# Performance work log

Measured on AMD Instinct MI355X. Metric: run time of the kernel, lower is better.

The kernel has to match this reference:

```python
import jax, jax.numpy as jnp
import numpy as np

B, T, D = 4, 1024, 1024
N_HEAD, HEAD, LATENT = 16, 64, 32
N_EXP, TOP_K, N_FF = 8, 2, 4096
HID = int(2 * N_FF / 3)  # 2730, Expert hidden when ffn_multiplier is None
CAP_FACTOR = 1.0


def setup_inputs() -> dict:
    key = jax.random.key(0)
    ks = jax.random.split(key, 14)
    s = 0.02
    f = lambda k, shp: jax.random.normal(k, shp, jnp.float32) * s
    return dict(
        x=jax.random.normal(ks[0], (B, T, D), jnp.float32),
        noise_eps=jax.random.normal(ks[1], (B, T, N_EXP), jnp.float32),
        ln1_w=jnp.ones((D,), jnp.float32),
        ln2_w=jnp.ones((D,), jnp.float32),
        q_w=f(ks[2], (N_HEAD, D, HEAD)), q_b=jnp.zeros((N_HEAD, HEAD), jnp.float32),
        ka_w=f(ks[3], (N_HEAD, D, LATENT)), kb_w=f(ks[4], (N_HEAD, LATENT, HEAD)),
        va_w=f(ks[5], (N_HEAD, D, LATENT)), vb_w=f(ks[6], (N_HEAD, LATENT, HEAD)),
        proj_w=f(ks[7], (D, D)), proj_b=jnp.zeros((D,), jnp.float32),
        route_w=f(ks[8], (D, N_EXP)), route_b=jnp.zeros((N_EXP,), jnp.float32),
        noise_w=f(ks[9], (D, N_EXP)), noise_b=jnp.zeros((N_EXP,), jnp.float32),
        swiglu_w=f(ks[10], (N_EXP, D, 2 * HID)),
        down_w=f(ks[11], (N_EXP, HID, D)),
    )


def _rms(x, w, eps=1e-5):
    x32 = x.astype(jnp.float32)
    n = x32 * jax.lax.rsqrt(jnp.mean(x32 * x32, -1, keepdims=True) + eps)
    return n.astype(x.dtype) * w


def _rope(q, k):
    # q,k: [B,H,T,hd]; even/odd split then concatenated halves (matches torch code)
    hd, Tq = q.shape[-1], q.shape[-2]
    inv = 1.0 / (10000.0 ** (jnp.arange(0, hd, 2, dtype=jnp.float32) / hd))
    ang = jnp.arange(Tq, dtype=jnp.float32)[:, None] * inv[None, :]  # [T, hd/2]
    cos, sin = jnp.cos(ang), jnp.sin(ang)
    def rot(t):
        t1, t2 = t[..., ::2], t[..., 1::2]
        return jnp.concatenate([t1 * cos - t2 * sin, t1 * sin + t2 * cos], -1)
    return rot(q), rot(k)


def reference(x, noise_eps, ln1_w, ln2_w, q_w, q_b, ka_w, kb_w, va_w, vb_w,
              proj_w, proj_b, route_w, route_b, noise_w, noise_b, swiglu_w, down_w):
    Bx, Tx, Dm = x.shape
    hd = q_w.shape[-1]
    E = route_w.shape[-1]
    # ---- Multi-Head Latent Attention (pre-norm) ----
    xn = _rms(x, ln1_w)
    q = jnp.einsum('btd,hde->bhte', xn, q_w) + q_b[None, :, None, :]
    k = jnp.einsum('bhtl,hle->bhte', jnp.einsum('btd,hdl->bhtl', xn, ka_w), kb_w)
    v = jnp.einsum('bhtl,hle->bhte', jnp.einsum('btd,hdl->bhtl', xn, va_w), vb_w)
    q, k = _rope(q, k)
    scores = jnp.einsum('bhtd,bhsd->bhts', q, k) / jnp.sqrt(jnp.float32(hd))
    attn = jax.nn.softmax(scores, axis=-1)  # NOTE: no causal mask in source
    o = jnp.einsum('bhts,bhsd->bhtd', attn, v)
    o = o.transpose(0, 2, 1, 3).reshape(Bx, Tx, Dm)
    x = x + (o @ proj_w + proj_b)
    # ---- Noisy top-k router ----
    xn2 = _rms(x, ln2_w)
    logits = xn2 @ route_w + route_b
    noisy = logits + noise_eps * jax.nn.softplus(xn2 @ noise_w + noise_b)  # temperature=1
    _, topi = jax.lax.top_k(noisy, TOP_K)  # [B,T,k]
    sel = jnp.any(jax.nn.one_hot(topi, E, dtype=jnp.bool_), axis=-2)  # [B,T,E]
    probs = jax.nn.softmax(jnp.where(sel, noisy, -jnp.inf), axis=-1)
    aux = jnp.sum((jnp.mean(probs, (0, 1)) - 1.0 / E) ** 2)
    # ---- Capacity-limited expert dispatch (first-come in flat token order) ----
    N = Bx * Tx
    cap = int(N * TOP_K / E * CAP_FACTOR)
    flat_x = xn2.reshape(N, Dm)
    flat_p = probs.reshape(N, E)
    flat_i = topi.reshape(N, TOP_K)
    upd = jnp.zeros((N, Dm), x.dtype)
    for e in range(E):
        m = jnp.any(flat_i == e, axis=-1)            # [N]
        pos = jnp.cumsum(m) - 1                      # slot within expert buffer
        keep = m & (pos < cap)
        slot = jnp.where(keep, pos, cap)             # dropped -> overflow slot
        tok = jnp.zeros(cap + 1, jnp.int32).at[slot].set(jnp.arange(N, dtype=jnp.int32))[:cap]
        valid = jnp.zeros(cap + 1, jnp.bool_).at[slot].set(keep)[:cap]
        xe = flat_x[tok] * valid[:, None]            # [cap, D]; zero rows yield zero output (no biases)
        h = xe @ swiglu_w[e]
        h1, h2 = jnp.split(h, 2, axis=-1)
        oe = (jax.nn.silu(h1) * h2) @ down_w[e]
        gate = jnp.where(valid, flat_p[tok, e], 0.0)
        upd = upd.at[tok].add(oe * gate[:, None])
    return x + upd.reshape(Bx, Tx, Dm), aux
```

## Files before the change

### kernel.cpp

```cpp
#include <hip/hip_runtime.h>
#include <math.h>

#define NTOK   4096
#define DM     1024
#define NHEAD  16
#define HDIM   64
#define NEXP   8
#define CAP    1024
#define HID    2730
#define NFF2   5460
#define HIDP   2752
#define KCD    86

typedef __attribute__((ext_vector_type(8))) short bf16x8;
typedef __attribute__((ext_vector_type(4))) float f32x4;
typedef __attribute__((ext_vector_type(8))) _Float16 h16x8;
typedef __attribute__((ext_vector_type(4))) _Float16 h16x4;
typedef __attribute__((ext_vector_type(8))) unsigned short u16x8;

__device__ __forceinline__ unsigned short f2bf(float f) {
  unsigned int u = __float_as_uint(f);
  u += 0x7fffu + ((u >> 16) & 1u);
  return (unsigned short)(u >> 16);
}

__device__ __forceinline__ void gll16(const void* g, void* l) {
  __builtin_amdgcn_global_load_lds((const __attribute__((address_space(1))) void*)g,
                                   (__attribute__((address_space(3))) void*)l, 16, 0, 0);
}

__global__ __launch_bounds__(256) void pack_dense3(const float* __restrict__ q_w,
                                                   const float* __restrict__ ka_w,
                                                   const float* __restrict__ va_w,
                                                   const float* __restrict__ proj_w,
                                                   unsigned short* __restrict__ Wqt,
                                                   unsigned short* __restrict__ Wlatt,
                                                   unsigned short* __restrict__ Wprojt) {
  int b = blockIdx.x;
  int tid = threadIdx.x;
  int col = tid & 63;
  int k0 = (tid >> 6) * 8;
  int which = b >> 9;
  int bb = b & 511;
  int nt = bb >> 5, kc = bb & 31;
  int d0 = kc * 32 + k0;
  u16x8 o;
  if (which == 0) {
    const float* src = q_w + ((size_t)nt * 1024 + d0) * 64 + col;
#pragma unroll
    for (int j = 0; j < 8; j++) o[j] = f2bf(src[(size_t)j * 64]);
    *(u16x8*)(Wqt + (size_t)bb * 2048 + tid * 8) = o;
  } else if (which == 1) {
    int n = nt * 64 + col;
    const float* base;
    int h, l;
    if (n < 512) { h = n >> 5; l = n & 31; base = ka_w; }
    else { int m = n - 512; h = m >> 5; l = m & 31; base = va_w; }
    const float* src = base + ((size_t)h * 1024 + d0) * 32 + l;
#pragma unroll
    for (int j = 0; j < 8; j++) o[j] = f2bf(src[(size_t)j * 32]);
    *(u16x8*)(Wlatt + (size_t)bb * 2048 + tid * 8) = o;
  } else {
    int n = nt * 64 + col;
    const float* src = proj_w + (size_t)d0 * 1024 + n;
#pragma unroll
    for (int j = 0; j < 8; j++) o[j] = f2bf(src[(size_t)j * 1024]);
    *(u16x8*)(Wprojt + (size_t)bb * 2048 + tid * 8) = o;
  }
}

__global__ __launch_bounds__(256) void pack_swiglu(const float* __restrict__ swiglu_w,
                                                   unsigned short* __restrict__ Wpk) {
  int b = blockIdx.x;
  int kc32 = b & 31;
  int ejt = b >> 5;
  int jt = ejt % 43;
  int e = ejt / 43;
  int tid = threadIdx.x;
  int col = tid & 63;
  int k0 = (tid >> 6) * 8;
  int n = jt * 64 + col;
  bool nv = n < HID;
  const float* src = swiglu_w + ((size_t)e * DM + kc32 * 32 + k0) * NFF2 + n;
  u16x8 o1, o2;
#pragma unroll
  for (int j = 0; j < 8; j++) {
    float v1 = nv ? src[(size_t)j * NFF2] : 0.f;
    float v2 = nv ? src[(size_t)j * NFF2 + HID] : 0.f;
    o1[j] = f2bf(v1);
    o2[j] = f2bf(v2);
  }
  unsigned short* dst = Wpk + (size_t)b * 4096 + tid * 8;
  *(u16x8*)dst = o1;
  *(u16x8*)(dst + 2048) = o2;
}

__global__ __launch_bounds__(256) void pack_down(const float* __restrict__ down_w,
                                                 unsigned short* __restrict__ Wdk) {
  int b = blockIdx.x;
  int kci = b % KCD;
  int ent = b / KCD;
  int nt = ent & 15;
  int e = ent >> 4;
  int tid = threadIdx.x;
  int col = tid & 63, k0 = (tid >> 6) * 8;
  int n = nt * 64 + col;
  int kbase = kci * 32 + k0;
  const float* src = down_w + ((size_t)e * HID + kbase) * DM + n;
  u16x8 o;
#pragma unroll
  for (int j = 0; j < 8; j++) {
    float v = (kbase + j < HID) ? src[(size_t)j * DM] : 0.f;
    o[j] = f2bf(v);
  }
  *(u16x8*)(Wdk + (size_t)b * 2048 + tid * 8) = o;
}

template <bool F32OUT>
__global__ __launch_bounds__(256) void rms_kernel(const float* __restrict__ x,
                                                  const float* __restrict__ w,
                                                  float* __restrict__ out,
                                                  unsigned short* __restrict__ outb) {
  int row = blockIdx.x;
  int tid = threadIdx.x;
  const float4 v = ((const float4*)(x + (size_t)row * DM))[tid];
  float ss = v.x * v.x + v.y * v.y + v.z * v.z + v.w * v.w;
#pragma unroll
  for (int off = 32; off >= 1; off >>= 1) ss += __shfl_down(ss, off);
  __shared__ float red[4];
  if ((tid & 63) == 0) red[tid >> 6] = ss;
  __syncthreads();
  float tot = red[0] + red[1] + red[2] + red[3];
  float scale = rsqrtf(tot * (1.0f / 1024.0f) + 1e-5f);
  const float4 wv = ((const float4*)w)[tid];
  float4 o;
  o.x = v.x * scale * wv.x; o.y = v.y * scale * wv.y;
  o.z = v.z * scale * wv.z; o.w = v.w * scale * wv.w;
  if (F32OUT) ((float4*)(out + (size_t)row * DM))[tid] = o;
  ushort4 ob;
  ob.x = f2bf(o.x); ob.y = f2bf(o.y); ob.z = f2bf(o.z); ob.w = f2bf(o.w);
  *(ushort4*)(outb + (size_t)row * DM + tid * 4) = ob;
}

template <bool BIAS, bool RES>
__global__ __launch_bounds__(256) void mfma_dense(const unsigned short* __restrict__ A,
                                                  const unsigned short* __restrict__ Bpk,
                                                  const float* __restrict__ bias,
                                                  const float* __restrict__ res,
                                                  float* __restrict__ C, int K, int N) {
  int m0 = blockIdx.x * 128;
  int n0 = blockIdx.y * 128;
  int KC = K >> 5;
  __shared__ unsigned short Asl[2][4096];
  __shared__ unsigned short Bsl[2][4096];
  int tid = threadIdx.x;
  int l6 = tid & 63, wid = tid >> 6;
  int lr = l6 & 15, lq = l6 >> 4;
  int wm0 = (wid >> 1) * 64, wn0 = (wid & 1) * 64;
  int aw = wid * 512;
  f32x4 c[4][4];
  f32x4 zz = {0.f, 0.f, 0.f, 0.f};
#pragma unroll
  for (int i = 0; i < 4; i++)
#pragma unroll
    for (int j = 0; j < 4; j++) c[i][j] = zz;
  const unsigned short* aAg = A + (size_t)(m0 + (tid & 127)) * K + (tid >> 7) * 8;
  const unsigned short* bg0 = Bpk + (size_t)((n0 >> 6) * KC) * 2048 + tid * 8;
  const unsigned short* bg1 = Bpk + (size_t)(((n0 >> 6) + 1) * KC) * 2048 + tid * 8;
#define DEN_STG(cur, kci)                                       \
  {                                                             \
    gll16(aAg + (kci) * 32, &Asl[cur][aw]);                     \
    gll16(aAg + (kci) * 32 + 16, &Asl[cur][2048 + aw]);         \
    gll16(bg0 + (size_t)(kci) * 2048, &Bsl[cur][aw]);           \
    gll16(bg1 + (size_t)(kci) * 2048, &Bsl[cur][2048 + aw]);    \
  }
  DEN_STG(0, 0);
  __syncthreads();
  for (int kci = 0; kci < KC; kci++) {
    int cur = kci & 1;
    if (kci + 1 < KC) DEN_STG(cur ^ 1, kci + 1);
    bf16x8 a[4], b[4];
#pragma unroll
    for (int mi = 0; mi < 4; mi++)
      a[mi] = *(bf16x8*)&Asl[cur][(lq * 128 + wm0 + mi * 16 + lr) * 8];
#pragma unroll
    for (int ni = 0; ni < 4; ni++)
      b[ni] = *(bf16x8*)&Bsl[cur][((wn0 >> 6) * 256 + lq * 64 + ni * 16 + lr) * 8];
#pragma unroll
    for (int mi = 0; mi < 4; mi++)
#pragma unroll
      for (int ni = 0; ni < 4; ni++)
        c[mi][ni] = __builtin_amdgcn_mfma_f32_16x16x32_bf16(a[mi], b[ni], c[mi][ni], 0, 0, 0);
    __syncthreads();
  }
#undef DEN_STG
#pragma unroll
  for (int mi = 0; mi < 4; mi++)
#pragma unroll
    for (int ni = 0; ni < 4; ni++) {
      int nn = n0 + wn0 + ni * 16 + lr;
      float bv = BIAS ? bias[nn] : 0.f;
#pragma unroll
      for (int r = 0; r < 4; r++) {
        int mm = m0 + wm0 + mi * 16 + lq * 4 + r;
        float v = c[mi][ni][r] + bv;
        if (RES) v += res[(size_t)mm * N + nn];
        C[(size_t)mm * N + nn] = v;
      }
    }
}

__global__ void expand_kernel(const float* __restrict__ latents, const float* __restrict__ kb_w,
                              const float* __restrict__ vb_w, float* __restrict__ kpre,
                              _Float16* __restrict__ vf) {
  int idx = blockIdx.x * 256 + threadIdx.x;
  int e = idx & 63;
  int t = (idx >> 6) & 1023;
  int h = (idx >> 16) & 15;
  int b = idx >> 20;
  const float* lrow = latents + ((size_t)(b * 1024 + t)) * DM;
  const float* kb = kb_w + (size_t)h * 2048;
  const float* vb = vb_w + (size_t)h * 2048;
  float ka = 0.f, va = 0.f;
#pragma unroll
  for (int l = 0; l < 32; l++) {
    ka += lrow[h * 32 + l] * kb[l * 64 + e];
    va += lrow[512 + h * 32 + l] * vb[l * 64 + e];
  }
  kpre[idx] = ka;
  vf[idx] = (_Float16)va;
}

template <bool IN_BTHD>
__global__ void rope_kernel(const float* __restrict__ in, _Float16* __restrict__ out) {
  int idx = blockIdx.x * 256 + threadIdx.x;
  int i = idx & 31;
  int t = (idx >> 5) & 1023;
  int h = (idx >> 15) & 15;
  int b = idx >> 19;
  size_t ib;
  if (IN_BTHD)
    ib = ((size_t)(b * 1024 + t)) * DM + h * 64;
  else
    ib = ((size_t)((b * 16 + h) * 1024 + t)) * 64;
  float t1 = in[ib + 2 * i], t2 = in[ib + 2 * i + 1];
  float inv = exp2f(-(float)i * 0.41524101186091903f);
  float ang = (float)t * inv;
  float s, c;
  sincosf(ang, &s, &c);
  size_t ob = ((size_t)((b * 16 + h) * 1024 + t)) * 64;
  out[ob + i] = (_Float16)(t1 * c - t2 * s);
  out[ob + 32 + i] = (_Float16)(t1 * s + t2 * c);
}

__global__ __launch_bounds__(256) void attn_mfma(const _Float16* __restrict__ qf,
                                                 const _Float16* __restrict__ kf,
                                                 const _Float16* __restrict__ vf,
                                                 unsigned short* __restrict__ o) {
  __shared__ _Float16 Ks[64][72];
  __shared__ _Float16 Vt[64][68];
  int bh = blockIdx.y;
  int q0 = blockIdx.x * 64;
  int tid = threadIdx.x;
  int wv = tid >> 6, lane = tid & 63;
  int lr = lane & 15, lq = lane >> 4;
  const size_t base = (size_t)bh * 1024 * 64;
  const _Float16* qrow = qf + base + (size_t)(q0 + wv * 16 + lr) * 64;
  h16x8 qfr[2];
  qfr[0] = *(const h16x8*)(qrow + lq * 8);
  qfr[1] = *(const h16x8*)(qrow + 32 + lq * 8);
  float mrow = -3.0e38f, lsum = 0.f;
  f32x4 oacc[4];
  f32x4 zz = {0.f, 0.f, 0.f, 0.f};
#pragma unroll
  for (int i = 0; i < 4; i++) oacc[i] = zz;
  int skey = tid >> 2, spart = tid & 3;
  int vkey = tid & 63, vdb = (tid >> 6) * 16;

  for (int kt = 0; kt < 16; kt++) {
    __syncthreads();
    {
      const _Float16* kg = kf + base + (size_t)(kt * 64 + skey) * 64 + spart * 16;
      *(h16x8*)&Ks[skey][spart * 16] = *(const h16x8*)kg;
      *(h16x8*)&Ks[skey][spart * 16 + 8] = *(const h16x8*)(kg + 8);
      const _Float16* vg = vf + base + (size_t)(kt * 64 + vkey) * 64 + vdb;
      h16x8 v0 = *(const h16x8*)vg;
      h16x8 v1 = *(const h16x8*)(vg + 8);
#pragma unroll
      for (int j = 0; j < 8; j++) {
        Vt[vdb + j][vkey] = v0[j];
        Vt[vdb + 8 + j][vkey] = v1[j];
      }
    }
    __syncthreads();
    f32x4 st[4];
#pragma unroll
    for (int ni = 0; ni < 4; ni++) {
      st[ni] = zz;
#pragma unroll
      for (int kc = 0; kc < 2; kc++) {
        h16x8 ak = *(const h16x8*)&Ks[ni * 16 + lr][kc * 32 + lq * 8];
        st[ni] = __builtin_amdgcn_mfma_f32_16x16x32_f16(ak, qfr[kc], st[ni], 0, 0, 0);
      }
    }
    float smax = -3.0e38f;
#pragma unroll
    for (int ni = 0; ni < 4; ni++)
#pragma unroll
      for (int r = 0; r < 4; r++) {
        st[ni][r] *= 0.125f;
        smax = fmaxf(smax, st[ni][r]);
      }
    smax = fmaxf(smax, __shfl_xor(smax, 16));
    smax = fmaxf(smax, __shfl_xor(smax, 32));
    float newm = fmaxf(mrow, smax);
    float alpha = expf(mrow - newm);
    float rsum = 0.f;
    h16x4 pf[4];
#pragma unroll
    for (int ni = 0; ni < 4; ni++)
#pragma unroll
      for (int r = 0; r < 4; r++) {
        float p = expf(st[ni][r] - newm);
        rsum += p;
        pf[ni][r] = (_Float16)p;
      }
    rsum += __shfl_xor(rsum, 16);
    rsum += __shfl_xor(rsum, 32);
    lsum = lsum * alpha + rsum;
    mrow = newm;
#pragma unroll
    for (int dt = 0; dt < 4; dt++) {
      oacc[dt][0] *= alpha; oacc[dt][1] *= alpha;
      oacc[dt][2] *= alpha; oacc[dt][3] *= alpha;
    }
#pragma unroll
    for (int dt = 0; dt < 4; dt++)
#pragma unroll
      for (int ni = 0; ni < 4; ni++) {
        h16x4 va = *(const h16x4*)&Vt[dt * 16 + lr][ni * 16 + lq * 4];
        oacc[dt] = __builtin_amdgcn_mfma_f32_16x16x16f16(va, pf[ni], oacc[dt], 0, 0, 0);
      }
  }
  int b = bh >> 4, h = bh & 15;
  int qg = q0 + wv * 16 + lr;
  float invl = 1.0f / lsum;
  unsigned short* orow = o + (size_t)(b * 1024 + qg) * DM + h * 64;
#pragma unroll
  for (int dt = 0; dt < 4; dt++) {
    ushort4 ov;
    ov.x = f2bf(oacc[dt][0] * invl);
    ov.y = f2bf(oacc[dt][1] * invl);
    ov.z = f2bf(oacc[dt][2] * invl);
    ov.w = f2bf(oacc[dt][3] * invl);
    *(ushort4*)(orow + dt * 16 + lq * 4) = ov;
  }
}

__global__ __launch_bounds__(256) void router_kernel(
    const float* __restrict__ xn2, const float* __restrict__ route_w,
    const float* __restrict__ route_b, const float* __restrict__ noise_w,
    const float* __restrict__ noise_b, const float* __restrict__ noise_eps,
    int* __restrict__ topi, float* __restrict__ flat_p, float* __restrict__ probsum,
    int* __restrict__ slotmap) {
  int wave = threadIdx.x >> 6;
  int lane = threadIdx.x & 63;
  int tk = blockIdx.x * 4 + wave;
  float acc[8] = {0.f}, nacc[8] = {0.f};
  const float* xr = xn2 + (size_t)tk * DM;
  for (int it = 0; it < 16; it++) {
    int d = it * 64 + lane;
    float xv = xr[d];
    const float* rw = route_w + d * 8;
    const float* nw = noise_w + d * 8;
#pragma unroll
    for (int e = 0; e < 8; e++) {
      acc[e] += xv * rw[e];
      nacc[e] += xv * nw[e];
    }
  }
#pragma unroll
  for (int off = 32; off >= 1; off >>= 1) {
#pragma unroll
    for (int e = 0; e < 8; e++) {
      acc[e] += __shfl_down(acc[e], off);
      nacc[e] += __shfl_down(nacc[e], off);
    }
  }
  if (lane == 0) {
    float noisy[8];
#pragma unroll
    for (int e = 0; e < 8; e++) {
      float lg = acc[e] + route_b[e];
      float nl = nacc[e] + noise_b[e];
      float sp = (nl > 20.f) ? nl : log1pf(expf(nl));
      noisy[e] = lg + noise_eps[tk * 8 + e] * sp;
    }
    int i1 = 0;
    float n1 = noisy[0];
#pragma unroll
    for (int e = 1; e < 8; e++)
      if (noisy[e] > n1) { n1 = noisy[e]; i1 = e; }
    int i2 = -1;
    float n2 = -3.0e38f;
#pragma unroll
    for (int e = 0; e < 8; e++)
      if (e != i1 && noisy[e] > n2) { n2 = noisy[e]; i2 = e; }
    float r = expf(n2 - n1);
    float p1 = 1.0f / (1.0f + r);
    float p2 = r / (1.0f + r);
    topi[tk * 2] = i1;
    topi[tk * 2 + 1] = i2;
#pragma unroll
    for (int e = 0; e < 8; e++) flat_p[tk * 8 + e] = (e == i1) ? p1 : ((e == i2) ? p2 : 0.f);
    atomicAdd(&probsum[i1], p1);
    atomicAdd(&probsum[i2], p2);
    slotmap[tk * 2] = -1;
    slotmap[tk * 2 + 1] = -1;
  }
}

__global__ __launch_bounds__(512) void scan_kernel(const int* __restrict__ topi,
                                                   const float* __restrict__ flat_p,
                                                   int* __restrict__ tok, float* __restrict__ gate,
                                                   int* __restrict__ cnt, int* __restrict__ slotmap) {
  int e = threadIdx.x >> 6;
  int lane = threadIdx.x & 63;
  int count = 0;
  for (int base = 0; base < NTOK; base += 64) {
    int t = base + lane;
    int a = topi[t * 2], b = topi[t * 2 + 1];
    bool mflag = (a == e) || (b == e);
    unsigned long long mask = __ballot(mflag);
    int pos = count + __popcll(mask & ((1ull << lane) - 1ull));
    if (mflag && pos < CAP) {
      tok[e * CAP + pos] = t;
      gate[e * CAP + pos] = flat_p[t * 8 + e];
      int k = (a == e) ? 0 : 1;
      slotmap[t * 2 + k] = pos;
    }
    count += __popcll(mask);
  }
  if (lane == 0) cnt[e] = (count < CAP) ? count : CAP;
}

__global__ __launch_bounds__(256) void mfma_swiglu(const unsigned short* __restrict__ xn2b,
                                                   const unsigned short* __restrict__ Wpk,
                                                   const int* __restrict__ tok,
                                                   const int* __restrict__ cnt,
                                                   unsigned short* __restrict__ ACT) {
  int L = blockIdx.x;
  int e = L & 7;
  int gw = L >> 3;
  int m0 = (gw & 7) * 128;
  int jt = gw >> 3;
  int j0 = jt * 64;
  __shared__ unsigned short Asl[2][4096];
  __shared__ unsigned short B1sl[2][2048];
  __shared__ unsigned short B2sl[2][2048];
  int tid = threadIdx.x;
  int l6 = tid & 63, wid = tid >> 6;
  int lr = l6 & 15, lq = l6 >> 4;
  int wm0 = (wid >> 1) * 64, wn0 = (wid & 1) * 32;
  int aw = wid * 512;
  int ce = cnt[e];
  int slot = m0 + (tid & 127);
  int tr = (slot < ce) ? tok[e * CAP + slot] : 0;
  const unsigned short* aAg = xn2b + (size_t)tr * DM + (tid >> 7) * 8;
  const unsigned short* wg = Wpk + (size_t)(e * 43 + jt) * 32 * 4096 + tid * 8;
  f32x4 c1[4][2], c2[4][2];
  f32x4 zz = {0.f, 0.f, 0.f, 0.f};
#pragma unroll
  for (int i = 0; i < 4; i++)
#pragma unroll
    for (int j = 0; j < 2; j++) { c1[i][j] = zz; c2[i][j] = zz; }
#define SWG_STG(cur, kci)                                        \
  {                                                              \
    gll16(aAg + (kci) * 32, &Asl[cur][aw]);                      \
    gll16(aAg + (kci) * 32 + 16, &Asl[cur][2048 + aw]);          \
    gll16(wg + (size_t)(kci) * 4096, &B1sl[cur][aw]);            \
    gll16(wg + (size_t)(kci) * 4096 + 2048, &B2sl[cur][aw]);     \
  }
  SWG_STG(0, 0);
  __syncthreads();
  for (int kci = 0; kci < 32; kci++) {
    int cur = kci & 1;
    if (kci + 1 < 32) SWG_STG(cur ^ 1, kci + 1);
    bf16x8 a[4], b1[2], b2[2];
#pragma unroll
    for (int mi = 0; mi < 4; mi++)
      a[mi] = *(bf16x8*)&Asl[cur][(lq * 128 + wm0 + mi * 16 + lr) * 8];
#pragma unroll
    for (int ni = 0; ni < 2; ni++) {
      b1[ni] = *(bf16x8*)&B1sl[cur][(lq * 64 + wn0 + ni * 16 + lr) * 8];
      b2[ni] = *(bf16x8*)&B2sl[cur][(lq * 64 + wn0 + ni * 16 + lr) * 8];
    }
#pragma unroll
    for (int mi = 0; mi < 4; mi++)
#pragma unroll
      for (int ni = 0; ni < 2; ni++) {
        c1[mi][ni] = __builtin_amdgcn_mfma_f32_16x16x32_bf16(a[mi], b1[ni], c1[mi][ni], 0, 0, 0);
        c2[mi][ni] = __builtin_amdgcn_mfma_f32_16x16x32_bf16(a[mi], b2[ni], c2[mi][ni], 0, 0, 0);
      }
    __syncthreads();
  }
#undef SWG_STG
#pragma unroll
  for (int mi = 0; mi < 4; mi++)
#pragma unroll
    for (int ni = 0; ni < 2; ni++)
#pragma unroll
      for (int r = 0; r < 4; r++) {
        int mm = m0 + wm0 + mi * 16 + lq * 4 + r;
        int cc = j0 + wn0 + ni * 16 + lr;
        float h1 = c1[mi][ni][r], h2 = c2[mi][ni][r];
        float act = (h1 / (1.0f + expf(-h1))) * h2;
        ACT[(size_t)e * CAP * HIDP + (size_t)mm * HIDP + cc] = f2bf(act);
      }
}

__global__ __launch_bounds__(256) void mfma_down(const unsigned short* __restrict__ ACT,
                                                 const unsigned short* __restrict__ Wdk,
                                                 float* __restrict__ OE) {
  int L = blockIdx.x;
  int e = L & 7;
  int gw = L >> 3;
  int m0 = (gw & 7) * 128;
  int nt0 = (gw >> 3) * 2;
  int n0 = nt0 * 64;
  __shared__ unsigned short Asl[2][4096];
  __shared__ unsigned short Bsl[2][4096];
  int tid = threadIdx.x;
  int l6 = tid & 63, wid = tid >> 6;
  int lr = l6 & 15, lq = l6 >> 4;
  int wm0 = (wid >> 1) * 64, wn0 = (wid & 1) * 64;
  int aw = wid * 512;
  f32x4 c[4][4];
  f32x4 zz = {0.f, 0.f, 0.f, 0.f};
#pragma unroll
  for (int i = 0; i < 4; i++)
#pragma unroll
    for (int j = 0; j < 4; j++) c[i][j] = zz;
  const unsigned short* aAg =
      ACT + (size_t)e * CAP * HIDP + (size_t)(m0 + (tid & 127)) * HIDP + (tid >> 7) * 8;
  const unsigned short* bg0 = Wdk + ((size_t)(e * 16 + nt0) * KCD) * 2048 + tid * 8;
  const unsigned short* bg1 = Wdk + ((size_t)(e * 16 + nt0 + 1) * KCD) * 2048 + tid * 8;
#define DWN_STG(cur, kci)                                       \
  {                                                             \
    gll16(aAg + (kci) * 32, &Asl[cur][aw]);                     \
    gll16(aAg + (kci) * 32 + 16, &Asl[cur][2048 + aw]);         \
    gll16(bg0 + (size_t)(kci) * 2048, &Bsl[cur][aw]);           \
    gll16(bg1 + (size_t)(kci) * 2048, &Bsl[cur][2048 + aw]);    \
  }
  DWN_STG(0, 0);
  __syncthreads();
  for (int kci = 0; kci < KCD; kci++) {
    int cur = kci & 1;
    if (kci + 1 < KCD) DWN_STG(cur ^ 1, kci + 1);
    bf16x8 a[4], b[4];
#pragma unroll
    for (int mi = 0; mi < 4; mi++)
      a[mi] = *(bf16x8*)&Asl[cur][(lq * 128 + wm0 + mi * 16 + lr) * 8];
#pragma unroll
    for (int ni = 0; ni < 4; ni++)
      b[ni] = *(bf16x8*)&Bsl[cur][((wn0 >> 6) * 256 + lq * 64 + ni * 16 + lr) * 8];
#pragma unroll
    for (int mi = 0; mi < 4; mi++)
#pragma unroll
      for (int ni = 0; ni < 4; ni++)
        c[mi][ni] = __builtin_amdgcn_mfma_f32_16x16x32_bf16(a[mi], b[ni], c[mi][ni], 0, 0, 0);
    __syncthreads();
  }
#undef DWN_STG
#pragma unroll
  for (int mi = 0; mi < 4; mi++)
#pragma unroll
    for (int ni = 0; ni < 4; ni++)
#pragma unroll
      for (int r = 0; r < 4; r++) {
        int mm = m0 + wm0 + mi * 16 + lq * 4 + r;
        int nn = n0 + wn0 + ni * 16 + lr;
        OE[((size_t)e << 20) + (size_t)mm * DM + nn] = c[mi][ni][r];
      }
}

__global__ void combine_kernel(const float* __restrict__ x2, const float* __restrict__ OE,
                               const int* __restrict__ topi, const int* __restrict__ slotmap,
                               const float* __restrict__ flat_p, float* __restrict__ out) {
  int idx = blockIdx.x * 256 + threadIdx.x;
  int t = idx >> 8;
  int c4 = (idx & 255) * 4;
  float4 v = *(const float4*)(x2 + (size_t)t * DM + c4);
#pragma unroll
  for (int k = 0; k < 2; k++) {
    int s = slotmap[t * 2 + k];
    if (s >= 0) {
      int e = topi[t * 2 + k];
      float g = flat_p[t * 8 + e];
      float4 ov = *(const float4*)(OE + ((size_t)e << 20) + (size_t)s * DM + c4);
      v.x += g * ov.x; v.y += g * ov.y; v.z += g * ov.z; v.w += g * ov.w;
    }
  }
  *(float4*)(out + (size_t)t * DM + c4) = v;
}

__global__ void aux_kernel(const float* __restrict__ probsum, float* __restrict__ out) {
  if (threadIdx.x == 0) {
    float s = 0.f;
#pragma unroll
    for (int e = 0; e < 8; e++) {
      float d = probsum[e] * (1.0f / 4096.0f) - 0.125f;
      s += d * d;
    }
    out[4194304] = s;
  }
}

extern "C" void kernel_launch(void* const* d_in, const int* in_sizes, int n_in, void* d_out,
                              int out_size, void* d_ws, size_t ws_size, hipStream_t stream) {
  const float* x = (const float*)d_in[0];
  const float* noise_eps = (const float*)d_in[1];
  const float* ln1_w = (const float*)d_in[2];
  const float* ln2_w = (const float*)d_in[3];
  const float* q_w = (const float*)d_in[4];
  const float* q_b = (const float*)d_in[5];
  const float* ka_w = (const float*)d_in[6];
  const float* kb_w = (const float*)d_in[7];
  const float* va_w = (const float*)d_in[8];
  const float* vb_w = (const float*)d_in[9];
  const float* proj_w = (const float*)d_in[10];
  const float* proj_b = (const float*)d_in[11];
  const float* route_w = (const float*)d_in[12];
  const float* route_b = (const float*)d_in[13];
  const float* noise_w = (const float*)d_in[14];
  const float* noise_b = (const float*)d_in[15];
  const float* swiglu_w = (const float*)d_in[16];
  const float* down_w = (const float*)d_in[17];
  float* out = (float*)d_out;
  char* w = (char*)d_ws;
  const size_t MB = 1ull << 20;

  float* x2 = (float*)(w + 0 * MB);
  float* xn2 = (float*)(w + 16 * MB);
  unsigned short* xn2b = (unsigned short*)(w + 32 * MB);
  char* sm = w + 40 * MB;
  unsigned short* xnb = (unsigned short*)(w + 42 * MB);
  float* qtmp = (float*)(w + 50 * MB);
  float* latents = (float*)(w + 66 * MB);
  float* kpre = (float*)(w + 82 * MB);
  _Float16* qfb = (_Float16*)(w + 98 * MB);
  _Float16* kfb = (_Float16*)(w + 106 * MB);
  _Float16* vfb = (_Float16*)(w + 114 * MB);
  unsigned short* obb = (unsigned short*)(w + 122 * MB);
  unsigned short* Wqt = (unsigned short*)(w + 130 * MB);
  unsigned short* Wlatt = (unsigned short*)(w + 132 * MB);
  unsigned short* Wprojt = (unsigned short*)(w + 134 * MB);
  unsigned short* Wpk = (unsigned short*)(w + 42 * MB);
  unsigned short* ACT = (unsigned short*)(w + 128 * MB);
  unsigned short* Wdk = (unsigned short*)(w + 42 * MB);
  float* OE = (float*)(w + 86 * MB);

  int* topi = (int*)sm;
  int* tok = (int*)(sm + 64 * 1024);
  int* cntb = (int*)(sm + 128 * 1024);
  int* slotmap = (int*)(sm + 192 * 1024);
  float* flat_p = (float*)(sm + 256 * 1024);
  float* gateb = (float*)(sm + 512 * 1024);
  float* probsum = (float*)(sm + 576 * 1024);

  pack_dense3<<<1536, 256, 0, stream>>>(q_w, ka_w, va_w, proj_w, Wqt, Wlatt, Wprojt);
  rms_kernel<false><<<4096, 256, 0, stream>>>(x, ln1_w, nullptr, xnb);
  mfma_dense<true, false><<<dim3(32, 8), 256, 0, stream>>>(xnb, Wqt, q_b, nullptr, qtmp, 1024, 1024);
  mfma_dense<false, false><<<dim3(32, 8), 256, 0, stream>>>(xnb, Wlatt, nullptr, nullptr, latents, 1024, 1024);
  expand_kernel<<<16384, 256, 0, stream>>>(latents, kb_w, vb_w, kpre, vfb);
  rope_kernel<true><<<8192, 256, 0, stream>>>(qtmp, qfb);
  rope_kernel<false><<<8192, 256, 0, stream>>>(kpre, kfb);
  attn_mfma<<<dim3(16, 64), 256, 0, stream>>>(qfb, kfb, vfb, obb);
  mfma_dense<true, true><<<dim3(32, 8), 256, 0, stream>>>(obb, Wprojt, proj_b, x, x2, 1024, 1024);
  pack_swiglu<<<11008, 256, 0, stream>>>(swiglu_w, Wpk);
  rms_kernel<true><<<4096, 256, 0, stream>>>(x2, ln2_w, xn2, xn2b);
  hipMemsetAsync(probsum, 0, 8 * sizeof(float), stream);
  router_kernel<<<1024, 256, 0, stream>>>(xn2, route_w, route_b, noise_w, noise_b, noise_eps,
                                          topi, flat_p, probsum, slotmap);
  scan_kernel<<<1, 512, 0, stream>>>(topi, flat_p, tok, gateb, cntb, slotmap);
  mfma_swiglu<<<2752, 256, 0, stream>>>(xn2b, Wpk, tok, cntb, ACT);
  pack_down<<<11008, 256, 0, stream>>>(down_w, Wdk);
  mfma_down<<<512, 256, 0, stream>>>(ACT, Wdk, OE);
  combine_kernel<<<4096, 256, 0, stream>>>(x2, OE, topi, slotmap, flat_p, out);
  aux_kernel<<<1, 64, 0, stream>>>(probsum, out);
}
```

Measured before the change: 966.2 us.

## Triple-buffer LDS staging with partial vmcnt waits in MFMA GEMM kernels

The dense, SwiGLU and down-projection GEMMs move from double-buffered to triple-buffered LDS staging. Loads run two k-steps ahead, and the full __syncthreads is replaced by s_waitcnt vmcnt(4) plus a raw s_barrier, so only the older stage's global-to-LDS loads must finish before the barrier. MFMA sections also raise wave priority with s_setprio. This is meant to hide global load latency better, at the cost of 50% more LDS per block, which may reduce occupancy.

```diff
diff --git a/kernel.cpp b/kernel.cpp
--- a/kernel.cpp
+++ b/kernel.cpp
@@ -28,6 +28,10 @@
   __builtin_amdgcn_global_load_lds((const __attribute__((address_space(1))) void*)g,
                                    (__attribute__((address_space(3))) void*)l, 16, 0, 0);
 }
+
+#define VM_WAIT4 asm volatile("s_waitcnt vmcnt(4)" ::: "memory")
+#define VM_WAIT0 asm volatile("s_waitcnt vmcnt(0)" ::: "memory")
+#define CFENCE   asm volatile("" ::: "memory")
 
 __global__ __launch_bounds__(256) void pack_dense3(const float* __restrict__ q_w,
                                                    const float* __restrict__ ka_w,
@@ -151,8 +155,8 @@
   int m0 = blockIdx.x * 128;
   int n0 = blockIdx.y * 128;
   int KC = K >> 5;
-  __shared__ unsigned short Asl[2][4096];
-  __shared__ unsigned short Bsl[2][4096];
+  __shared__ unsigned short Asl[3][4096];
+  __shared__ unsigned short Bsl[3][4096];
   int tid = threadIdx.x;
   int l6 = tid & 63, wid = tid >> 6;
   int lr = l6 & 15, lq = l6 >> 4;
@@ -167,31 +171,42 @@
   const unsigned short* aAg = A + (size_t)(m0 + (tid & 127)) * K + (tid >> 7) * 8;
   const unsigned short* bg0 = Bpk + (size_t)((n0 >> 6) * KC) * 2048 + tid * 8;
   const unsigned short* bg1 = Bpk + (size_t)(((n0 >> 6) + 1) * KC) * 2048 + tid * 8;
-#define DEN_STG(cur, kci)                                       \
+#define DEN_STG(buf, kci)                                       \
   {                                                             \
-    gll16(aAg + (kci) * 32, &Asl[cur][aw]);                     \
-    gll16(aAg + (kci) * 32 + 16, &Asl[cur][2048 + aw]);         \
-    gll16(bg0 + (size_t)(kci) * 2048, &Bsl[cur][aw]);           \
-    gll16(bg1 + (size_t)(kci) * 2048, &Bsl[cur][2048 + aw]);    \
+    gll16(aAg + (kci) * 32, &Asl[buf][aw]);                     \
+    gll16(aAg + (kci) * 32 + 16, &Asl[buf][2048 + aw]);         \
+    gll16(bg0 + (size_t)(kci) * 2048, &Bsl[buf][aw]);           \
+    gll16(bg1 + (size_t)(kci) * 2048, &Bsl[buf][2048 + aw]);    \
   }
   DEN_STG(0, 0);
-  __syncthreads();
+  DEN_STG(1, 1);
+  VM_WAIT4;
+  __builtin_amdgcn_s_barrier();
+  CFENCE;
+  int rb = 0, sb = 2;
   for (int kci = 0; kci < KC; kci++) {
-    int cur = kci & 1;
-    if (kci + 1 < KC) DEN_STG(cur ^ 1, kci + 1);
     bf16x8 a[4], b[4];
 #pragma unroll
     for (int mi = 0; mi < 4; mi++)
-      a[mi] = *(bf16x8*)&Asl[cur][(lq * 128 + wm0 + mi * 16 + lr) * 8];
+      a[mi] = *(bf16x8*)&Asl[rb][(lq * 128 + wm0 + mi * 16 + lr) * 8];
 #pragma unroll
     for (int ni = 0; ni < 4; ni++)
-      b[ni] = *(bf16x8*)&Bsl[cur][((wn0 >> 6) * 256 + lq * 64 + ni * 16 + lr) * 8];
+      b[ni] = *(bf16x8*)&Bsl[rb][((wn0 >> 6) * 256 + lq * 64 + ni * 16 + lr) * 8];
+    if (kci + 2 < KC) DEN_STG(sb, kci + 2);
+    __builtin_amdgcn_s_setprio(1);
 #pragma unroll
     for (int mi = 0; mi < 4; mi++)
 #pragma unroll
       for (int ni = 0; ni < 4; ni++)
         c[mi][ni] = __builtin_amdgcn_mfma_f32_16x16x32_bf16(a[mi], b[ni], c[mi][ni], 0, 0, 0);
-    __syncthreads();
+    __builtin_amdgcn_s_setprio(0);
+    if (kci + 1 < KC) {
+      if (kci + 2 < KC) { VM_WAIT4; } else { VM_WAIT0; }
+      __builtin_amdgcn_s_barrier();
+      CFENCE;
+    }
+    rb = (rb == 2) ? 0 : rb + 1;
+    sb = (sb == 2) ? 0 : sb + 1;
   }
 #undef DEN_STG
 #pragma unroll
@@ -455,9 +470,9 @@
   int m0 = (gw & 7) * 128;
   int jt = gw >> 3;
   int j0 = jt * 64;
-  __shared__ unsigned short Asl[2][4096];
-  __shared__ unsigned short B1sl[2][2048];
-  __shared__ unsigned short B2sl[2][2048];
+  __shared__ unsigned short Asl[3][4096];
+  __shared__ unsigned short B1sl[3][2048];
+  __shared__ unsigned short B2sl[3][2048];
   int tid = threadIdx.x;
   int l6 = tid & 63, wid = tid >> 6;
   int lr = l6 & 15, lq = l6 >> 4;
@@ -474,27 +489,31 @@
   for (int i = 0; i < 4; i++)
 #pragma unroll
     for (int j = 0; j < 2; j++) { c1[i][j] = zz; c2[i][j] = zz; }
-#define SWG_STG(cur, kci)                                        \
+#define SWG_STG(buf, kci)                                        \
   {                                                              \
-    gll16(aAg + (kci) * 32, &Asl[cur][aw]);                      \
-    gll16(aAg + (kci) * 32 + 16, &Asl[cur][2048 + aw]);          \
-    gll16(wg + (size_t)(kci) * 4096, &B1sl[cur][aw]);            \
-    gll16(wg + (size_t)(kci) * 4096 + 2048, &B2sl[cur][aw]);     \
+    gll16(aAg + (kci) * 32, &Asl[buf][aw]);                      \
+    gll16(aAg + (kci) * 32 + 16, &Asl[buf][2048 + aw]);          \
+    gll16(wg + (size_t)(kci) * 4096, &B1sl[buf][aw]);            \
+    gll16(wg + (size_t)(kci) * 4096 + 2048, &B2sl[buf][aw]);     \
   }
   SWG_STG(0, 0);
-  __syncthreads();
+  SWG_STG(1, 1);
+  VM_WAIT4;
+  __builtin_amdgcn_s_barrier();
+  CFENCE;
+  int rb = 0, sb = 2;
   for (int kci = 0; kci < 32; kci++) {
-    int cur = kci & 1;
-    if (kci + 1 < 32) SWG_STG(cur ^ 1, kci + 1);
     bf16x8 a[4], b1[2], b2[2];
 #pragma unroll
     for (int mi = 0; mi < 4; mi++)
-      a[mi] = *(bf16x8*)&Asl[cur][(lq * 128 + wm0 + mi * 16 + lr) * 8];
+      a[mi] = *(bf16x8*)&Asl[rb][(lq * 128 + wm0 + mi * 16 + lr) * 8];
 #pragma unroll
     for (int ni = 0; ni < 2; ni++) {
-      b1[ni] = *(bf16x8*)&B1sl[cur][(lq * 64 + wn0 + ni * 16 + lr) * 8];
-      b2[ni] = *(bf16x8*)&B2sl[cur][(lq * 64 + wn0 + ni * 16 + lr) * 8];
-    }
+      b1[ni] = *(bf16x8*)&B1sl[rb][(lq * 64 + wn0 + ni * 16 + lr) * 8];
+      b2[ni] = *(bf16x8*)&B2sl[rb][(lq * 64 + wn0 + ni * 16 + lr) * 8];
+    }
+    if (kci + 2 < 32) SWG_STG(sb, kci + 2);
+    __builtin_amdgcn_s_setprio(1);
 #pragma unroll
     for (int mi = 0; mi < 4; mi++)
 #pragma unroll
@@ -502,7 +521,14 @@
         c1[mi][ni] = __builtin_amdgcn_mfma_f32_16x16x32_bf16(a[mi], b1[ni], c1[mi][ni], 0, 0, 0);
         c2[mi][ni] = __builtin_amdgcn_mfma_f32_16x16x32_bf16(a[mi], b2[ni], c2[mi][ni], 0, 0, 0);
       }
-    __syncthreads();
+    __builtin_amdgcn_s_setprio(0);
+    if (kci + 1 < 32) {
+      if (kci + 2 < 32) { VM_WAIT4; } else { VM_WAIT0; }
+      __builtin_amdgcn_s_barrier();
+      CFENCE;
+    }
+    rb = (rb == 2) ? 0 : rb + 1;
+    sb = (sb == 2) ? 0 : sb + 1;
   }
 #undef SWG_STG
 #pragma unroll
@@ -528,8 +554,8 @@
   int m0 = (gw & 7) * 128;
   int nt0 = (gw >> 3) * 2;
   int n0 = nt0 * 64;
-  __shared__ unsigned short Asl[2][4096];
-  __shared__ unsigned short Bsl[2][4096];
+  __shared__ unsigned short Asl[3][4096];
+  __shared__ unsigned short Bsl[3][4096];
   int tid = threadIdx.x;
   int l6 = tid & 63, wid = tid >> 6;
   int lr = l6 & 15, lq = l6 >> 4;
@@ -545,31 +571,42 @@
       ACT + (size_t)e * CAP * HIDP + (size_t)(m0 + (tid & 127)) * HIDP + (tid >> 7) * 8;
   const unsigned short* bg0 = Wdk + ((size_t)(e * 16 + nt0) * KCD) * 2048 + tid * 8;
   const unsigned short* bg1 = Wdk + ((size_t)(e * 16 + nt0 + 1) * KCD) * 2048 + tid * 8;
-#define DWN_STG(cur, kci)                                       \
+#define DWN_STG(buf, kci)                                       \
   {                                                             \
-    gll16(aAg + (kci) * 32, &Asl[cur][aw]);                     \
-    gll16(aAg + (kci) * 32 + 16, &Asl[cur][2048 + aw]);         \
-    gll16(bg0 + (size_t)(kci) * 2048, &Bsl[cur][aw]);           \
-    gll16(bg1 + (size_t)(kci) * 2048, &Bsl[cur][2048 + aw]);    \
+    gll16(aAg + (kci) * 32, &Asl[buf][aw]);                     \
+    gll16(aAg + (kci) * 32 + 16, &Asl[buf][2048 + aw]);         \
+    gll16(bg0 + (size_t)(kci) * 2048, &Bsl[buf][aw]);           \
+    gll16(bg1 + (size_t)(kci) * 2048, &Bsl[buf][2048 + aw]);    \
   }
   DWN_STG(0, 0);
-  __syncthreads();
+  DWN_STG(1, 1);
+  VM_WAIT4;
+  __builtin_amdgcn_s_barrier();
+  CFENCE;
+  int rb = 0, sb = 2;
   for (int kci = 0; kci < KCD; kci++) {
-    int cur = kci & 1;
-    if (kci + 1 < KCD) DWN_STG(cur ^ 1, kci + 1);
     bf16x8 a[4], b[4];
 #pragma unroll
     for (int mi = 0; mi < 4; mi++)
-      a[mi] = *(bf16x8*)&Asl[cur][(lq * 128 + wm0 + mi * 16 + lr) * 8];
+      a[mi] = *(bf16x8*)&Asl[rb][(lq * 128 + wm0 + mi * 16 + lr) * 8];
 #pragma unroll
     for (int ni = 0; ni < 4; ni++)
-      b[ni] = *(bf16x8*)&Bsl[cur][((wn0 >> 6) * 256 + lq * 64 + ni * 16 + lr) * 8];
+      b[ni] = *(bf16x8*)&Bsl[rb][((wn0 >> 6) * 256 + lq * 64 + ni * 16 + lr) * 8];
+    if (kci + 2 < KCD) DWN_STG(sb, kci + 2);
+    __builtin_amdgcn_s_setprio(1);
 #pragma unroll
     for (int mi = 0; mi < 4; mi++)
 #pragma unroll
       for (int ni = 0; ni < 4; ni++)
         c[mi][ni] = __builtin_amdgcn_mfma_f32_16x16x32_bf16(a[mi], b[ni], c[mi][ni], 0, 0, 0);
-    __syncthreads();
+    __builtin_amdgcn_s_setprio(0);
+    if (kci + 1 < KCD) {
+      if (kci + 2 < KCD) { VM_WAIT4; } else { VM_WAIT0; }
+      __builtin_amdgcn_s_barrier();
+      CFENCE;
+    }
+    rb = (rb == 2) ? 0 : rb + 1;
+    sb = (sb == 2) ? 0 : sb + 1;
   }
 #undef DWN_STG
 #pragma unroll
```

Result: faster. 922.7 us (-4.5%).
